# Kernel tuning notes

Hardware: AMD Instinct MI355X
Metric: run time of the kernel (lower is better)

## Reference

```python
import math
import jax, jax.numpy as jnp
import numpy as np

DIM = 1024
QK_DIM = 200
HIDDEN = 2 * DIM  # expansion_factor = 2
N = 8192


def setup_inputs() -> dict:
    key = jax.random.key(0)
    ks = jax.random.split(key, 8)
    s = 0.02
    return {
        "x": jax.random.normal(ks[0], (N, DIM), dtype=jnp.float32),
        "W_hidden": jax.random.normal(ks[1], (DIM, 2 * HIDDEN), dtype=jnp.float32) * s,
        "b_hidden": jnp.zeros((2 * HIDDEN,), dtype=jnp.float32),
        "W_qk": jax.random.normal(ks[2], (DIM, QK_DIM), dtype=jnp.float32) * s,
        "b_qk": jnp.zeros((QK_DIM,), dtype=jnp.float32),
        "gamma": 1.0 + jax.random.normal(ks[3], (2, QK_DIM), dtype=jnp.float32) * s,
        "beta": jnp.zeros((2, QK_DIM), dtype=jnp.float32),
        "W_out": jax.random.normal(ks[4], (HIDDEN, DIM), dtype=jnp.float32) * s,
        "b_out": jnp.zeros((DIM,), dtype=jnp.float32),
    }


def reference(x, W_hidden, b_hidden, W_qk, b_qk, gamma, beta, W_out, b_out):
    # to_hidden: Linear(dim -> 2*hidden) + SiLU, then chunk into v, gate
    hid = jax.nn.silu(x @ W_hidden + b_hidden)        # [N, 2H]
    v, gate = jnp.split(hid, 2, axis=-1)              # [N, H] each
    # to_qk: Linear(dim -> qk_dim) + SiLU
    qk = jax.nn.silu(x @ W_qk + b_qk)                 # [N, qk]
    # OffsetScale (heads=2): per-head affine on the shared qk
    q = qk * gamma[0] + beta[0]                       # [N, qk]
    k = qk * gamma[1] + beta[1]                       # [N, qk]
    # scores scaled by sqrt(dim) (module uses self.dim, not qk_dim)
    sim = (q @ k.T) * (1.0 / math.sqrt(x.shape[-1]))  # [N, N]
    # ReLU-squared attention (no softmax); dropout=0.0 -> identity
    attn = jnp.square(jax.nn.relu(sim))
    out = attn @ v                                    # [N, H]
    out = out * gate
    out = out @ W_out + b_out                         # [N, dim]
    # add_residual=True in this module multiplies by x
    return out * x
```

## Files before the change

kernel.cpp:

```cpp
#include <hip/hip_runtime.h>
#include <stdint.h>


typedef __bf16 bf16x8 __attribute__((ext_vector_type(8)));
typedef float f32x4 __attribute__((ext_vector_type(4)));

__device__ __forceinline__ uint16_t f2bf(float f) {
  uint32_t u = __builtin_bit_cast(uint32_t, f);
  u += 0x7fffu + ((u >> 16) & 1u);
  return (uint16_t)(u >> 16);
}
__device__ __forceinline__ float silu_f(float s) {
  return s / (1.f + __expf(-s));
}

__device__ __forceinline__ void gload16(const void* g, void* l) {
  __builtin_amdgcn_global_load_lds(
      (__attribute__((address_space(1))) void*)const_cast<void*>(g),
      (__attribute__((address_space(3))) void*)l, 16, 0, 0);
}


__global__ void cast_to_bf16(const float* __restrict__ in, uint16_t* __restrict__ out, int n4) {
  int i = blockIdx.x * blockDim.x + threadIdx.x;
  if (i < n4) {
    float4 f = ((const float4*)in)[i];
    ushort4 o;
    o.x = f2bf(f.x); o.y = f2bf(f.y); o.z = f2bf(f.z); o.w = f2bf(f.w);
    ((ushort4*)out)[i] = o;
  }
}

__global__ void transpose_cast_pad(const float* __restrict__ in, uint16_t* __restrict__ out,
                                   int R, int C, int Cp) {
  __shared__ float tile[32][33];
  int cb = blockIdx.x * 32;
  int rb = blockIdx.y * 32;
  int tx = threadIdx.x;
  int ty = threadIdx.y;
#pragma unroll
  for (int i = 0; i < 4; ++i) {
    int r = rb + ty + i * 8;
    int c = cb + tx;
    tile[ty + i * 8][tx] = (c < C) ? in[(size_t)r * C + c] : 0.f;
  }
  __syncthreads();
#pragma unroll
  for (int i = 0; i < 4; ++i) {
    int c = cb + ty + i * 8;
    if (c < Cp) out[(size_t)c * R + rb + tx] = f2bf(tile[tx][ty + i * 8]);
  }
}

__global__ void k_sum(uint16_t* __restrict__ P0, const uint16_t* __restrict__ P1,
                      const uint16_t* __restrict__ g, int n8) {
  int i = blockIdx.x * blockDim.x + threadIdx.x;
  if (i < n8) {
    bf16x8 a = ((const bf16x8*)P0)[i];
    bf16x8 b = ((const bf16x8*)P1)[i];
    bf16x8 gg = ((const bf16x8*)g)[i];
    bf16x8 o;
#pragma unroll
    for (int e = 0; e < 8; ++e)
      o[e] = (__bf16)(((float)a[e] + (float)b[e]) * (float)gg[e]);
    ((bf16x8*)P0)[i] = o;
  }
}


struct EpiParams {
  const float* bias;
  const float* bias2;
  const float* g0;
  const float* b0;
  const float* g1;
  const float* b1;
  const uint16_t* gate;
  const float* x;
  uint16_t* o16a;
  uint16_t* o16b;
  uint16_t* oq;
  uint16_t* ok;
  float* o32;
};

#define TILE128(T_, B_, BS_)                                                   \
  do {                                                                         \
    const uint16_t* base_ = SH + (B_) * 8192;                                  \
    const int kp_ = (((T_) + 3) & (NT - 1)) * 32;                              \
    uint16_t* sd_ = SH + (BS_) * 8192 + wave * 512;                            \
    gload16(gA0 + kp_, sd_);                                                   \
    gload16(gA1 + kp_, sd_ + 2048);                                            \
    gload16(gB0 + kp_, sd_ + 4096);                                            \
    gload16(gB1 + kp_, sd_ + 6144);                                            \
    bf16x8 a_[4], b_[4];                                                       \
    _Pragma("unroll") for (int j = 0; j < 4; ++j)                              \
        b_[j] = *(const bf16x8*)(base_ + rdB + j * 512);                       \
    _Pragma("unroll") for (int i = 0; i < 4; ++i)                              \
        a_[i] = *(const bf16x8*)(base_ + rdA + i * 512);                       \
    __builtin_amdgcn_s_setprio(1);                                             \
    _Pragma("unroll") for (int i = 0; i < 4; ++i)                              \
      _Pragma("unroll") for (int j = 0; j < 4; ++j)                            \
          acc[i][j] = __builtin_amdgcn_mfma_f32_16x16x32_bf16(                 \
              a_[i], b_[j], acc[i][j], 0, 0, 0);                               \
    __builtin_amdgcn_s_setprio(0);                                             \
    asm volatile("s_waitcnt vmcnt(8)" ::: "memory");                           \
    __builtin_amdgcn_sched_barrier(0);                                         \
    __builtin_amdgcn_s_barrier();                                              \
    __builtin_amdgcn_sched_barrier(0);                                         \
  } while (0)

#define RING_LOOP128()                                                         \
  do {                                                                         \
    _Pragma("unroll") for (int s_ = 0; s_ < 3; ++s_) {                         \
      uint16_t* d_ = SH + s_ * 8192 + wave * 512;                              \
      gload16(gA0 + s_ * 32, d_);                                              \
      gload16(gA1 + s_ * 32, d_ + 2048);                                       \
      gload16(gB0 + s_ * 32, d_ + 4096);                                       \
      gload16(gB1 + s_ * 32, d_ + 6144);                                       \
    }                                                                          \
    asm volatile("s_waitcnt vmcnt(8)" ::: "memory");                           \
    __builtin_amdgcn_sched_barrier(0);                                         \
    __builtin_amdgcn_s_barrier();                                              \
    __builtin_amdgcn_sched_barrier(0);                                         \
    for (int t0_ = 0; t0_ < NT; t0_ += 4) {                                    \
      TILE128(t0_ + 0, 0, 3);                                                  \
      TILE128(t0_ + 1, 1, 0);                                                  \
      TILE128(t0_ + 2, 2, 1);                                                  \
      TILE128(t0_ + 3, 3, 2);                                                  \
    }                                                                          \
    asm volatile("s_waitcnt vmcnt(0)" ::: "memory");                           \
    __builtin_amdgcn_sched_barrier(0);                                         \
    __syncthreads();                                                           \
  } while (0)

__global__ __launch_bounds__(256, 2) void k_hidqk(
    const uint16_t* __restrict__ A, const uint16_t* __restrict__ Bt, EpiParams p) {
  __shared__ __align__(16) uint16_t SH[32768];

  const int tid = threadIdx.x;
  const int lane = tid & 63;
  const int wave = tid >> 6;
  const int wr = (wave >> 1) * 64;
  const int wc = (wave & 1) * 64;
  const int m0 = blockIdx.y * 128;
  const int n0 = blockIdx.x * 128;
  const int lda = 1024, ldb = 1024;
  const int NT = 32;

  f32x4 acc[4][4] = {};

  const int fr = lane & 15;
  const int rg = lane >> 4;
  const int swz = (rg ^ ((fr >> 1) & 3)) * 8;
  const int rdA = (wr + fr) * 32 + swz;
  const int rdB = 4096 + (wc + fr) * 32 + swz;

  const int srow = lane >> 2;
  const int sk = ((lane & 3) ^ ((lane >> 3) & 3)) * 8;
  const uint16_t* gA0 = A + (size_t)(m0 + wave * 16 + srow) * lda + sk;
  const uint16_t* gA1 = gA0 + (size_t)64 * lda;
  const uint16_t* gB0 = Bt + (size_t)(n0 + wave * 16 + srow) * ldb + sk;
  const uint16_t* gB1 = gB0 + (size_t)64 * ldb;

  RING_LOOP128();

  if (n0 < 2048) {
    uint16_t* ar = SH + wave * 2048;
    const int lrow = lane >> 3;
    const int mc = (lane & 7) * 8;
#pragma unroll
    for (int j = 0; j < 4; ++j) {
      const float bc = p.bias[n0 + wc + j * 16 + fr];
#pragma unroll
      for (int i = 0; i < 4; ++i)
#pragma unroll
        for (int r = 0; r < 4; ++r)
          ar[fr * 72 + i * 16 + rg * 4 + r] = f2bf(silu_f(acc[i][j][r] + bc));
#pragma unroll
      for (int rr = 0; rr < 2; ++rr) {
        bf16x8 v = *(const bf16x8*)(ar + (rr * 8 + lrow) * 72 + mc);
        *(bf16x8*)(p.o16a + (size_t)(n0 + wc + j * 16 + rr * 8 + lrow) * 8192 + m0 + wr + mc) = v;
      }
    }
  } else if (n0 < 4096) {
    uint16_t* ar = SH + wave * 2048;
    const int lrow = lane >> 3;
    const int nc = (lane & 7) * 8;
    float bc[4];
#pragma unroll
    for (int j = 0; j < 4; ++j) bc[j] = p.bias[n0 + wc + j * 16 + fr];
#pragma unroll
    for (int i = 0; i < 4; ++i) {
#pragma unroll
      for (int j = 0; j < 4; ++j)
#pragma unroll
        for (int r = 0; r < 4; ++r)
          ar[(rg * 4 + r) * 72 + j * 16 + fr] = f2bf(silu_f(acc[i][j][r] + bc[j]));
#pragma unroll
      for (int rr = 0; rr < 2; ++rr) {
        bf16x8 v = *(const bf16x8*)(ar + (rr * 8 + lrow) * 72 + nc);
        *(bf16x8*)(p.o16b + (size_t)(m0 + wr + i * 16 + rr * 8 + lrow) * 2048 + (n0 - 2048) + wc + nc) = v;
      }
    }
  } else {
#pragma unroll
    for (int i = 0; i < 4; ++i) {
#pragma unroll
      for (int j = 0; j < 4; ++j) {
        const int row = m0 + wr + i * 16 + rg * 4;
        const int qc = n0 + wc + j * 16 + fr - 4096;
#pragma unroll
        for (int r = 0; r < 4; ++r) {
          float qv = 0.f, kv = 0.f;
          if (qc < 200) {
            float s = silu_f(acc[i][j][r] + p.bias2[qc]);
            qv = s * p.g0[qc] + p.b0[qc];
            kv = s * p.g1[qc] + p.b1[qc];
          }
          p.oq[(size_t)(row + r) * 256 + qc] = f2bf(qv);
          p.ok[(size_t)(row + r) * 256 + qc] = f2bf(kv);
        }
      }
    }
  }
}

__global__ __launch_bounds__(256, 2) void k_attn(
    const uint16_t* __restrict__ Q,
    const uint16_t* __restrict__ Kt,
    uint16_t* __restrict__ attn) {
  __shared__ __align__(16) uint16_t SH[32768];

  const int tid = threadIdx.x;
  const int lane = tid & 63;
  const int wave = tid >> 6;
  const int wr = (wave >> 1) * 64;
  const int wc = (wave & 1) * 64;
  const int m0 = blockIdx.y * 128;
  const int n0 = blockIdx.x * 128;
  const int lda = 256, ldb = 256;
  const int NT = 8;

  f32x4 acc[4][4] = {};

  const int fr = lane & 15;
  const int rg = lane >> 4;
  const int swz = (rg ^ ((fr >> 1) & 3)) * 8;
  const int rdA = (wr + fr) * 32 + swz;
  const int rdB = 4096 + (wc + fr) * 32 + swz;

  const int srow = lane >> 2;
  const int sk = ((lane & 3) ^ ((lane >> 3) & 3)) * 8;
  const uint16_t* gA0 = Q + (size_t)(m0 + wave * 16 + srow) * lda + sk;
  const uint16_t* gA1 = gA0 + (size_t)64 * lda;
  const uint16_t* gB0 = Kt + (size_t)(n0 + wave * 16 + srow) * ldb + sk;
  const uint16_t* gB1 = gB0 + (size_t)64 * ldb;

  RING_LOOP128();

#pragma unroll
  for (int i = 0; i < 4; ++i) {
    uint16_t* sl = SH + wave * 4096 + (i & 1) * 2048;
#pragma unroll
    for (int j = 0; j < 4; ++j)
#pragma unroll
      for (int r = 0; r < 4; ++r) {
        float s = fmaxf(acc[i][j][r] * 0.03125f, 0.f);
        sl[(rg * 4 + r) * 72 + j * 16 + fr] = f2bf(s * s);
      }
    const int row = lane >> 2;
    const int c0 = (lane & 3) * 16;
    bf16x8 v0 = *(const bf16x8*)(sl + row * 72 + c0);
    bf16x8 v1 = *(const bf16x8*)(sl + row * 72 + c0 + 8);
    uint16_t* dst = attn + (size_t)(m0 + wr + i * 16 + row) * 8192 + (n0 + wc + c0);
    *(bf16x8*)(dst) = v0;
    *(bf16x8*)(dst + 8) = v1;
  }
}

__global__ __launch_bounds__(512, 2) void k_pv(
    const uint16_t* __restrict__ A,
    const uint16_t* __restrict__ Bt,
    uint16_t* __restrict__ P0,
    uint16_t* __restrict__ P1) {
  __shared__ __align__(16) uint16_t SH[65536];

  const int id = blockIdx.x;
  const int bx = id & 7;
  const int kh = (id >> 3) & 1;
  const int by = id >> 4;
  const int m0 = by * 256;
  const int n0 = bx * 256;
  const int kv0 = kh * 4096;

  const int tid = threadIdx.x;
  const int lane = tid & 63;
  const int wave = tid >> 6;
  const int wrM = (wave >> 2) * 128;
  const int wcN = (wave & 3) * 64;

  const int fr = lane & 15;
  const int rg = lane >> 4;
  const int swz = (rg ^ ((fr >> 1) & 3)) * 8;

  const int rdA = (wrM + fr) * 32 + swz;
  const int rdB = 8192 + (wcN + fr) * 32 + swz;

  const int srow = lane >> 2;
  const int sk = ((lane & 3) ^ ((lane >> 3) & 3)) * 8;
  const uint16_t* gA0 = A + (size_t)(m0 + wave * 16 + srow) * 8192 + kv0 + sk;
  const uint16_t* gA1 = gA0 + (size_t)128 * 8192;
  const uint16_t* gB0 = Bt + (size_t)(n0 + wave * 16 + srow) * 8192 + kv0 + sk;
  const uint16_t* gB1 = gB0 + (size_t)128 * 8192;

  f32x4 acc[8][4] = {};
  const int NT = 128;

  for (int s = 0; s < 3; ++s) {
    const int ko = s * 32;
    uint16_t* d = SH + s * 16384 + wave * 512;
    gload16(gA0 + ko, d);
    gload16(gA1 + ko, d + 4096);
    gload16(gB0 + ko, d + 8192);
    gload16(gB1 + ko, d + 12288);
  }
  asm volatile("s_waitcnt vmcnt(8)" ::: "memory");
  __builtin_amdgcn_sched_barrier(0);
  __builtin_amdgcn_s_barrier();
  __builtin_amdgcn_sched_barrier(0);

#define PV_TILE(T_, B_, BS_)                                                   \
  do {                                                                         \
    const uint16_t* bA_ = SH + (B_) * 16384;                                   \
    const int kp_ = (((T_) + 3) & (NT - 1)) * 32;                              \
    uint16_t* sd_ = SH + (BS_) * 16384 + wave * 512;                           \
    gload16(gA0 + kp_, sd_);                                                   \
    gload16(gA1 + kp_, sd_ + 4096);                                            \
    gload16(gB0 + kp_, sd_ + 8192);                                            \
    gload16(gB1 + kp_, sd_ + 12288);                                           \
    bf16x8 aq[8], bq[4];                                                       \
    _Pragma("unroll") for (int j = 0; j < 4; ++j)                              \
        bq[j] = *(const bf16x8*)(bA_ + rdB + j * 512);                         \
    _Pragma("unroll") for (int i = 0; i < 8; ++i)                              \
        aq[i] = *(const bf16x8*)(bA_ + rdA + i * 512);                         \
    __builtin_amdgcn_s_setprio(1);                                             \
    _Pragma("unroll") for (int i = 0; i < 8; ++i)                              \
      _Pragma("unroll") for (int j = 0; j < 4; ++j)                            \
          acc[i][j] = __builtin_amdgcn_mfma_f32_16x16x32_bf16(                 \
              aq[i], bq[j], acc[i][j], 0, 0, 0);                               \
    __builtin_amdgcn_s_setprio(0);                                             \
    asm volatile("s_waitcnt vmcnt(8)" ::: "memory");                           \
    __builtin_amdgcn_sched_barrier(0);                                         \
    __builtin_amdgcn_s_barrier();                                              \
    __builtin_amdgcn_sched_barrier(0);                                         \
  } while (0)

  for (int t0 = 0; t0 < NT; t0 += 4) {
    PV_TILE(t0 + 0, 0, 3);
    PV_TILE(t0 + 1, 1, 0);
    PV_TILE(t0 + 2, 2, 1);
    PV_TILE(t0 + 3, 3, 2);
  }
#undef PV_TILE

  asm volatile("s_waitcnt vmcnt(0)" ::: "memory");
  __builtin_amdgcn_sched_barrier(0);
  __builtin_amdgcn_s_barrier();
  __builtin_amdgcn_sched_barrier(0);

  uint16_t* dst = kh ? P1 : P0;
  uint16_t* ar = SH + wave * 2048;
  const int lrow = lane >> 3;
  const int nc = (lane & 7) * 8;
#pragma unroll
  for (int i = 0; i < 8; ++i) {
#pragma unroll
    for (int j = 0; j < 4; ++j)
#pragma unroll
      for (int r = 0; r < 4; ++r)
        ar[(rg * 4 + r) * 72 + j * 16 + fr] = f2bf(acc[i][j][r]);
#pragma unroll
    for (int rr = 0; rr < 2; ++rr) {
      const size_t base = (size_t)(m0 + wrM + i * 16 + rr * 8 + lrow) * 2048 + n0 + wcN + nc;
      bf16x8 v = *(const bf16x8*)(ar + (rr * 8 + lrow) * 72 + nc);
      *(bf16x8*)(dst + base) = v;
    }
  }
}

__global__ __launch_bounds__(256, 2) void k_final(
    const uint16_t* __restrict__ A,
    const uint16_t* __restrict__ Bt, EpiParams p) {
  __shared__ __align__(16) uint16_t SH[32768];

  const int tid = threadIdx.x;
  const int lane = tid & 63;
  const int wave = tid >> 6;
  const int wr = (wave >> 1) * 64;
  const int wc = (wave & 1) * 64;
  const int m0 = blockIdx.y * 128;
  const int n0 = blockIdx.x * 128;
  const int lda = 2048, ldb = 2048;
  const int NT = 64;

  f32x4 acc[4][4] = {};

  const int fr = lane & 15;
  const int rg = lane >> 4;
  const int swz = (rg ^ ((fr >> 1) & 3)) * 8;
  const int rdA = (wr + fr) * 32 + swz;
  const int rdB = 4096 + (wc + fr) * 32 + swz;

  const int srow = lane >> 2;
  const int sk = ((lane & 3) ^ ((lane >> 3) & 3)) * 8;
  const uint16_t* gA0 = A + (size_t)(m0 + wave * 16 + srow) * lda + sk;
  const uint16_t* gA1 = gA0 + (size_t)64 * lda;
  const uint16_t* gB0 = Bt + (size_t)(n0 + wave * 16 + srow) * ldb + sk;
  const uint16_t* gB1 = gB0 + (size_t)64 * ldb;

  RING_LOOP128();

#pragma unroll
  for (int i = 0; i < 4; ++i) {
#pragma unroll
    for (int j = 0; j < 4; ++j) {
      const int row = m0 + wr + i * 16 + rg * 4;
      const int col = n0 + wc + j * 16 + fr;
      const float bc = p.bias[col];
#pragma unroll
      for (int r = 0; r < 4; ++r) {
        size_t idx = (size_t)(row + r) * 1024 + col;
        p.o32[idx] = (acc[i][j][r] + bc) * p.x[idx];
      }
    }
  }
}


extern "C" void kernel_launch(void* const* d_in, const int* in_sizes, int n_in,
                              void* d_out, int out_size, void* d_ws, size_t ws_size,
                              hipStream_t stream) {
  const float* x        = (const float*)d_in[0];
  const float* W_hidden = (const float*)d_in[1];
  const float* b_hidden = (const float*)d_in[2];
  const float* W_qk     = (const float*)d_in[3];
  const float* b_qk     = (const float*)d_in[4];
  const float* gamma    = (const float*)d_in[5];
  const float* beta     = (const float*)d_in[6];
  const float* W_out    = (const float*)d_in[7];
  const float* b_out    = (const float*)d_in[8];
  float* out = (float*)d_out;

  char* base = (char*)d_ws;
  uint16_t* xb    = (uint16_t*)(base);
  uint16_t* WhT   = (uint16_t*)(base + (16ull << 20));
  uint16_t* WqkT  = (uint16_t*)(base + (24ull << 20));
  uint16_t* attnB = (uint16_t*)(base);
  char* tail = base + (64ull << 20);
  uint16_t* WoT   = (uint16_t*)(tail);
  uint16_t* q     = (uint16_t*)(tail + (4ull << 20));
  uint16_t* kk    = (uint16_t*)(tail + (8ull << 20));
  uint16_t* vT    = (uint16_t*)(tail + (12ull << 20));
  uint16_t* gate  = (uint16_t*)(tail + (44ull << 20));
  uint16_t* out2g = (uint16_t*)(tail + (76ull << 20));
  (void)in_sizes; (void)n_in; (void)out_size; (void)ws_size;

  const size_t PH = 4096ull * 2048;

  cast_to_bf16<<<(8192 * 1024 / 4) / 256, 256, 0, stream>>>(x, xb, 8192 * 1024 / 4);
  transpose_cast_pad<<<dim3(4096 / 32, 1024 / 32), dim3(32, 8), 0, stream>>>(W_hidden, WhT, 1024, 4096, 4096);
  transpose_cast_pad<<<dim3(256 / 32, 1024 / 32), dim3(32, 8), 0, stream>>>(W_qk, WqkT, 1024, 200, 256);
  transpose_cast_pad<<<dim3(1024 / 32, 2048 / 32), dim3(32, 8), 0, stream>>>(W_out, WoT, 2048, 1024, 1024);

  {
    EpiParams p{};
    p.bias = b_hidden; p.bias2 = b_qk;
    p.g0 = gamma; p.b0 = beta; p.g1 = gamma + 200; p.b1 = beta + 200;
    p.o16a = vT; p.o16b = gate; p.oq = q; p.ok = kk;
    k_hidqk<<<dim3(34, 64), 256, 0, stream>>>(xb, WhT, p);
  }

  for (int s = 0; s < 2; ++s) {
    k_attn<<<dim3(64, 32), 256, 0, stream>>>(q + (size_t)s * 4096 * 256, kk, attnB);

    uint16_t* Pa = out2g + (size_t)s * PH;
    uint16_t* Pb = out2g + (size_t)(1 - s) * PH;
    k_pv<<<dim3(256), 512, 0, stream>>>(attnB, vT, Pa, Pb);

    k_sum<<<dim3((int)(PH / 8 / 256)), 256, 0, stream>>>(
        Pa, Pb, gate + (size_t)s * PH, (int)(PH / 8));

    EpiParams p{};
    p.bias = b_out;
    p.x = x + (size_t)s * 4096 * 1024;
    p.o32 = out + (size_t)s * 4096 * 1024;
    k_final<<<dim3(8, 32), 256, 0, stream>>>(Pa, WoT, p);
  }
}
```

Baseline: 653.5 us.

## Use 256x256 register-double-buffered GEMM engine and full-M attention path

Introduces a shared 256x256-tile GEMM main loop that double-buffers LDS fragments in registers, so the LDS reads for the next k-step overlap with the current MFMAs. k_hidqk and k_attn move from 128x128 tiles to this engine. When the workspace is large enough, the whole 8192x8192 attention matrix is computed in one pass and PV runs without the K-split, with the gate multiply fused into the PV epilogue, removing k_sum and the per-half launches. The cost is more registers and LDS per block and a dependence on workspace size to pick the path.

```diff
diff --git a/kernel.cpp b/kernel.cpp
--- a/kernel.cpp
+++ b/kernel.cpp
@@ -84,6 +84,60 @@
   float* o32;
 };
 
+#define ET(T_, WS_, RS_, CA_, CB_, NA_, NB_)                                   \
+  do {                                                                         \
+    const int kp_ = (((T_) + 3) & (NT - 1)) * 32;                              \
+    uint16_t* sd_ = SH + (WS_) * 16384 + wave * 512;                           \
+    gload16(gA0 + kp_, sd_);                                                   \
+    gload16(gA1 + kp_, sd_ + 4096);                                            \
+    gload16(gB0 + kp_, sd_ + 8192);                                            \
+    gload16(gB1 + kp_, sd_ + 12288);                                           \
+    const uint16_t* rb_ = SH + (RS_) * 16384;                                  \
+    _Pragma("unroll") for (int j_ = 0; j_ < 4; ++j_)                           \
+        NB_[j_] = *(const bf16x8*)(rb_ + rdB + j_ * 512);                      \
+    _Pragma("unroll") for (int i_ = 0; i_ < 8; ++i_)                           \
+        NA_[i_] = *(const bf16x8*)(rb_ + rdA + i_ * 512);                      \
+    __builtin_amdgcn_sched_barrier(0);                                         \
+    __builtin_amdgcn_s_setprio(1);                                             \
+    _Pragma("unroll") for (int i_ = 0; i_ < 8; ++i_)                           \
+      _Pragma("unroll") for (int j_ = 0; j_ < 4; ++j_)                         \
+          acc[i_][j_] = __builtin_amdgcn_mfma_f32_16x16x32_bf16(               \
+              CA_[i_], CB_[j_], acc[i_][j_], 0, 0, 0);                         \
+    __builtin_amdgcn_s_setprio(0);                                             \
+    asm volatile("s_waitcnt vmcnt(4)" ::: "memory");                           \
+    __builtin_amdgcn_sched_barrier(0);                                         \
+    __builtin_amdgcn_s_barrier();                                              \
+    __builtin_amdgcn_sched_barrier(0);                                         \
+  } while (0)
+
+#define ENGINE256()                                                            \
+  do {                                                                         \
+    _Pragma("unroll") for (int s_ = 0; s_ < 3; ++s_) {                         \
+      uint16_t* d_ = SH + s_ * 16384 + wave * 512;                             \
+      gload16(gA0 + s_ * 32, d_);                                              \
+      gload16(gA1 + s_ * 32, d_ + 4096);                                       \
+      gload16(gB0 + s_ * 32, d_ + 8192);                                       \
+      gload16(gB1 + s_ * 32, d_ + 12288);                                      \
+    }                                                                          \
+    asm volatile("s_waitcnt vmcnt(4)" ::: "memory");                           \
+    __builtin_amdgcn_sched_barrier(0);                                         \
+    __builtin_amdgcn_s_barrier();                                              \
+    __builtin_amdgcn_sched_barrier(0);                                         \
+    _Pragma("unroll") for (int j_ = 0; j_ < 4; ++j_)                           \
+        fb0[j_] = *(const bf16x8*)(SH + rdB + j_ * 512);                       \
+    _Pragma("unroll") for (int i_ = 0; i_ < 8; ++i_)                           \
+        fa0[i_] = *(const bf16x8*)(SH + rdA + i_ * 512);                       \
+    for (int t0_ = 0; t0_ < NT; t0_ += 4) {                                    \
+      ET(t0_ + 0, 3, 1, fa0, fb0, fa1, fb1);                                   \
+      ET(t0_ + 1, 0, 2, fa1, fb1, fa0, fb0);                                   \
+      ET(t0_ + 2, 1, 3, fa0, fb0, fa1, fb1);                                   \
+      ET(t0_ + 3, 2, 0, fa1, fb1, fa0, fb0);                                   \
+    }                                                                          \
+    asm volatile("s_waitcnt vmcnt(0)" ::: "memory");                           \
+    __builtin_amdgcn_sched_barrier(0);                                         \
+    __syncthreads();                                                           \
+  } while (0)
+
 #define TILE128(T_, B_, BS_)                                                   \
   do {                                                                         \
     const uint16_t* base_ = SH + (B_) * 8192;                                  \
@@ -94,15 +148,15 @@
     gload16(gB0 + kp_, sd_ + 4096);                                            \
     gload16(gB1 + kp_, sd_ + 6144);                                            \
     bf16x8 a_[4], b_[4];                                                       \
-    _Pragma("unroll") for (int j = 0; j < 4; ++j)                              \
-        b_[j] = *(const bf16x8*)(base_ + rdB + j * 512);                       \
-    _Pragma("unroll") for (int i = 0; i < 4; ++i)                              \
-        a_[i] = *(const bf16x8*)(base_ + rdA + i * 512);                       \
+    _Pragma("unroll") for (int j_ = 0; j_ < 4; ++j_)                           \
+        b_[j_] = *(const bf16x8*)(base_ + rdB + j_ * 512);                     \
+    _Pragma("unroll") for (int i_ = 0; i_ < 4; ++i_)                           \
+        a_[i_] = *(const bf16x8*)(base_ + rdA + i_ * 512);                     \
     __builtin_amdgcn_s_setprio(1);                                             \
-    _Pragma("unroll") for (int i = 0; i < 4; ++i)                              \
-      _Pragma("unroll") for (int j = 0; j < 4; ++j)                            \
-          acc[i][j] = __builtin_amdgcn_mfma_f32_16x16x32_bf16(                 \
-              a_[i], b_[j], acc[i][j], 0, 0, 0);                               \
+    _Pragma("unroll") for (int i_ = 0; i_ < 4; ++i_)                           \
+      _Pragma("unroll") for (int j_ = 0; j_ < 4; ++j_)                         \
+          acc[i_][j_] = __builtin_amdgcn_mfma_f32_16x16x32_bf16(               \
+              a_[i_], b_[j_], acc[i_][j_], 0, 0, 0);                           \
     __builtin_amdgcn_s_setprio(0);                                             \
     asm volatile("s_waitcnt vmcnt(8)" ::: "memory");                           \
     __builtin_amdgcn_sched_barrier(0);                                         \
@@ -134,53 +188,54 @@
     __syncthreads();                                                           \
   } while (0)
 
-__global__ __launch_bounds__(256, 2) void k_hidqk(
+__global__ __launch_bounds__(512, 2) void k_hidqk(
     const uint16_t* __restrict__ A, const uint16_t* __restrict__ Bt, EpiParams p) {
-  __shared__ __align__(16) uint16_t SH[32768];
+  __shared__ __align__(16) uint16_t SH[65536];
 
   const int tid = threadIdx.x;
   const int lane = tid & 63;
   const int wave = tid >> 6;
-  const int wr = (wave >> 1) * 64;
-  const int wc = (wave & 1) * 64;
-  const int m0 = blockIdx.y * 128;
-  const int n0 = blockIdx.x * 128;
+  const int wrM = (wave >> 2) * 128;
+  const int wcN = (wave & 3) * 64;
+  const int m0 = blockIdx.y * 256;
+  const int n0 = blockIdx.x * 256;
   const int lda = 1024, ldb = 1024;
   const int NT = 32;
 
-  f32x4 acc[4][4] = {};
+  f32x4 acc[8][4] = {};
 
   const int fr = lane & 15;
   const int rg = lane >> 4;
   const int swz = (rg ^ ((fr >> 1) & 3)) * 8;
-  const int rdA = (wr + fr) * 32 + swz;
-  const int rdB = 4096 + (wc + fr) * 32 + swz;
+  const int rdA = (wrM + fr) * 32 + swz;
+  const int rdB = 8192 + (wcN + fr) * 32 + swz;
 
   const int srow = lane >> 2;
   const int sk = ((lane & 3) ^ ((lane >> 3) & 3)) * 8;
   const uint16_t* gA0 = A + (size_t)(m0 + wave * 16 + srow) * lda + sk;
-  const uint16_t* gA1 = gA0 + (size_t)64 * lda;
+  const uint16_t* gA1 = gA0 + (size_t)128 * lda;
   const uint16_t* gB0 = Bt + (size_t)(n0 + wave * 16 + srow) * ldb + sk;
-  const uint16_t* gB1 = gB0 + (size_t)64 * ldb;
-
-  RING_LOOP128();
+  const uint16_t* gB1 = gB0 + (size_t)128 * ldb;
+
+  bf16x8 fa0[8], fb0[4], fa1[8], fb1[4];
+  ENGINE256();
 
   if (n0 < 2048) {
-    uint16_t* ar = SH + wave * 2048;
-    const int lrow = lane >> 3;
-    const int mc = (lane & 7) * 8;
+    uint16_t* ar = SH + wave * 2304;
 #pragma unroll
     for (int j = 0; j < 4; ++j) {
-      const float bc = p.bias[n0 + wc + j * 16 + fr];
-#pragma unroll
-      for (int i = 0; i < 4; ++i)
+      const float bc = p.bias[n0 + wcN + j * 16 + fr];
+#pragma unroll
+      for (int i = 0; i < 8; ++i)
 #pragma unroll
         for (int r = 0; r < 4; ++r)
-          ar[fr * 72 + i * 16 + rg * 4 + r] = f2bf(silu_f(acc[i][j][r] + bc));
-#pragma unroll
-      for (int rr = 0; rr < 2; ++rr) {
-        bf16x8 v = *(const bf16x8*)(ar + (rr * 8 + lrow) * 72 + mc);
-        *(bf16x8*)(p.o16a + (size_t)(n0 + wc + j * 16 + rr * 8 + lrow) * 8192 + m0 + wr + mc) = v;
+          ar[fr * 136 + i * 16 + rg * 4 + r] = f2bf(silu_f(acc[i][j][r] + bc));
+      const int mc = (lane & 15) * 8;
+#pragma unroll
+      for (int it = 0; it < 4; ++it) {
+        const int nrow = it * 4 + (lane >> 4);
+        bf16x8 v = *(const bf16x8*)(ar + nrow * 136 + mc);
+        *(bf16x8*)(p.o16a + (size_t)(n0 + wcN + j * 16 + nrow) * 8192 + m0 + wrM + mc) = v;
       }
     }
   } else if (n0 < 4096) {
@@ -189,9 +244,9 @@
     const int nc = (lane & 7) * 8;
     float bc[4];
 #pragma unroll
-    for (int j = 0; j < 4; ++j) bc[j] = p.bias[n0 + wc + j * 16 + fr];
-#pragma unroll
-    for (int i = 0; i < 4; ++i) {
+    for (int j = 0; j < 4; ++j) bc[j] = p.bias[n0 + wcN + j * 16 + fr];
+#pragma unroll
+    for (int i = 0; i < 8; ++i) {
 #pragma unroll
       for (int j = 0; j < 4; ++j)
 #pragma unroll
@@ -200,16 +255,16 @@
 #pragma unroll
       for (int rr = 0; rr < 2; ++rr) {
         bf16x8 v = *(const bf16x8*)(ar + (rr * 8 + lrow) * 72 + nc);
-        *(bf16x8*)(p.o16b + (size_t)(m0 + wr + i * 16 + rr * 8 + lrow) * 2048 + (n0 - 2048) + wc + nc) = v;
+        *(bf16x8*)(p.o16b + (size_t)(m0 + wrM + i * 16 + rr * 8 + lrow) * 2048 + (n0 - 2048) + wcN + nc) = v;
       }
     }
   } else {
 #pragma unroll
-    for (int i = 0; i < 4; ++i) {
+    for (int i = 0; i < 8; ++i) {
 #pragma unroll
       for (int j = 0; j < 4; ++j) {
-        const int row = m0 + wr + i * 16 + rg * 4;
-        const int qc = n0 + wc + j * 16 + fr - 4096;
+        const int row = m0 + wrM + i * 16 + rg * 4;
+        const int qc = wcN + j * 16 + fr;
 #pragma unroll
         for (int r = 0; r < 4; ++r) {
           float qv = 0.f, kv = 0.f;
@@ -226,84 +281,97 @@
   }
 }
 
-__global__ __launch_bounds__(256, 2) void k_attn(
+__global__ __launch_bounds__(512, 2) void k_attn(
     const uint16_t* __restrict__ Q,
     const uint16_t* __restrict__ Kt,
     uint16_t* __restrict__ attn) {
-  __shared__ __align__(16) uint16_t SH[32768];
-
-  const int tid = threadIdx.x;
-  const int lane = tid & 63;
-  const int wave = tid >> 6;
-  const int wr = (wave >> 1) * 64;
-  const int wc = (wave & 1) * 64;
-  const int m0 = blockIdx.y * 128;
-  const int n0 = blockIdx.x * 128;
-  const int lda = 256, ldb = 256;
-  const int NT = 8;
-
-  f32x4 acc[4][4] = {};
-
-  const int fr = lane & 15;
-  const int rg = lane >> 4;
-  const int swz = (rg ^ ((fr >> 1) & 3)) * 8;
-  const int rdA = (wr + fr) * 32 + swz;
-  const int rdB = 4096 + (wc + fr) * 32 + swz;
-
-  const int srow = lane >> 2;
-  const int sk = ((lane & 3) ^ ((lane >> 3) & 3)) * 8;
-  const uint16_t* gA0 = Q + (size_t)(m0 + wave * 16 + srow) * lda + sk;
-  const uint16_t* gA1 = gA0 + (size_t)64 * lda;
-  const uint16_t* gB0 = Kt + (size_t)(n0 + wave * 16 + srow) * ldb + sk;
-  const uint16_t* gB1 = gB0 + (size_t)64 * ldb;
-
-  RING_LOOP128();
-
-#pragma unroll
-  for (int i = 0; i < 4; ++i) {
-    uint16_t* sl = SH + wave * 4096 + (i & 1) * 2048;
-#pragma unroll
-    for (int j = 0; j < 4; ++j)
-#pragma unroll
-      for (int r = 0; r < 4; ++r) {
-        float s = fmaxf(acc[i][j][r] * 0.03125f, 0.f);
-        sl[(rg * 4 + r) * 72 + j * 16 + fr] = f2bf(s * s);
-      }
-    const int row = lane >> 2;
-    const int c0 = (lane & 3) * 16;
-    bf16x8 v0 = *(const bf16x8*)(sl + row * 72 + c0);
-    bf16x8 v1 = *(const bf16x8*)(sl + row * 72 + c0 + 8);
-    uint16_t* dst = attn + (size_t)(m0 + wr + i * 16 + row) * 8192 + (n0 + wc + c0);
-    *(bf16x8*)(dst) = v0;
-    *(bf16x8*)(dst + 8) = v1;
-  }
-}
-
-__global__ __launch_bounds__(512, 2) void k_pv(
-    const uint16_t* __restrict__ A,
-    const uint16_t* __restrict__ Bt,
-    uint16_t* __restrict__ P0,
-    uint16_t* __restrict__ P1) {
   __shared__ __align__(16) uint16_t SH[65536];
-
-  const int id = blockIdx.x;
-  const int bx = id & 7;
-  const int kh = (id >> 3) & 1;
-  const int by = id >> 4;
-  const int m0 = by * 256;
-  const int n0 = bx * 256;
-  const int kv0 = kh * 4096;
 
   const int tid = threadIdx.x;
   const int lane = tid & 63;
   const int wave = tid >> 6;
   const int wrM = (wave >> 2) * 128;
   const int wcN = (wave & 3) * 64;
+  const int m0 = blockIdx.y * 256;
+  const int n0 = blockIdx.x * 256;
+  const int lda = 256, ldb = 256;
+  const int NT = 8;
+
+  f32x4 acc[8][4] = {};
 
   const int fr = lane & 15;
   const int rg = lane >> 4;
   const int swz = (rg ^ ((fr >> 1) & 3)) * 8;
-
+  const int rdA = (wrM + fr) * 32 + swz;
+  const int rdB = 8192 + (wcN + fr) * 32 + swz;
+
+  const int srow = lane >> 2;
+  const int sk = ((lane & 3) ^ ((lane >> 3) & 3)) * 8;
+  const uint16_t* gA0 = Q + (size_t)(m0 + wave * 16 + srow) * lda + sk;
+  const uint16_t* gA1 = gA0 + (size_t)128 * lda;
+  const uint16_t* gB0 = Kt + (size_t)(n0 + wave * 16 + srow) * ldb + sk;
+  const uint16_t* gB1 = gB0 + (size_t)128 * ldb;
+
+  bf16x8 fa0[8], fb0[4], fa1[8], fb1[4];
+  ENGINE256();
+
+  uint16_t* ar = SH + wave * 2048;
+  const int row = lane >> 2;
+  const int c0 = (lane & 3) * 16;
+#pragma unroll
+  for (int i = 0; i < 8; ++i) {
+#pragma unroll
+    for (int j = 0; j < 4; ++j)
+#pragma unroll
+      for (int r = 0; r < 4; ++r) {
+        float s = fmaxf(acc[i][j][r] * 0.03125f, 0.f);
+        ar[(rg * 4 + r) * 72 + j * 16 + fr] = f2bf(s * s);
+      }
+    bf16x8 v0 = *(const bf16x8*)(ar + row * 72 + c0);
+    bf16x8 v1 = *(const bf16x8*)(ar + row * 72 + c0 + 8);
+    uint16_t* dst = attn + (size_t)(m0 + wrM + i * 16 + row) * 8192 + (n0 + wcN + c0);
+    *(bf16x8*)(dst) = v0;
+    *(bf16x8*)(dst + 8) = v1;
+  }
+}
+
+__global__ __launch_bounds__(512, 2) void k_pv(
+    const uint16_t* __restrict__ A,
+    const uint16_t* __restrict__ Bt,
+    uint16_t* __restrict__ P0,
+    uint16_t* __restrict__ P1,
+    const uint16_t* __restrict__ gate,
+    int split) {
+  __shared__ __align__(16) uint16_t SH[65536];
+
+  const int id = blockIdx.x;
+  int bx, by, kv0, NT;
+  uint16_t* dst;
+  if (split) {
+    bx = id & 7;
+    by = id >> 4;
+    kv0 = ((id >> 3) & 1) * 4096;
+    NT = 128;
+    dst = ((id >> 3) & 1) ? P1 : P0;
+  } else {
+    bx = (id >> 3) & 7;
+    by = (id & 7) + 8 * (id >> 6);
+    kv0 = 0;
+    NT = 256;
+    dst = P0;
+  }
+  const int m0 = by * 256;
+  const int n0 = bx * 256;
+
+  const int tid = threadIdx.x;
+  const int lane = tid & 63;
+  const int wave = tid >> 6;
+  const int wrM = (wave >> 2) * 128;
+  const int wcN = (wave & 3) * 64;
+
+  const int fr = lane & 15;
+  const int rg = lane >> 4;
+  const int swz = (rg ^ ((fr >> 1) & 3)) * 8;
   const int rdA = (wrM + fr) * 32 + swz;
   const int rdB = 8192 + (wcN + fr) * 32 + swz;
 
@@ -315,61 +383,9 @@
   const uint16_t* gB1 = gB0 + (size_t)128 * 8192;
 
   f32x4 acc[8][4] = {};
-  const int NT = 128;
-
-  for (int s = 0; s < 3; ++s) {
-    const int ko = s * 32;
-    uint16_t* d = SH + s * 16384 + wave * 512;
-    gload16(gA0 + ko, d);
-    gload16(gA1 + ko, d + 4096);
-    gload16(gB0 + ko, d + 8192);
-    gload16(gB1 + ko, d + 12288);
-  }
-  asm volatile("s_waitcnt vmcnt(8)" ::: "memory");
-  __builtin_amdgcn_sched_barrier(0);
-  __builtin_amdgcn_s_barrier();
-  __builtin_amdgcn_sched_barrier(0);
-
-#define PV_TILE(T_, B_, BS_)                                                   \
-  do {                                                                         \
-    const uint16_t* bA_ = SH + (B_) * 16384;                                   \
-    const int kp_ = (((T_) + 3) & (NT - 1)) * 32;                              \
-    uint16_t* sd_ = SH + (BS_) * 16384 + wave * 512;                           \
-    gload16(gA0 + kp_, sd_);                                                   \
-    gload16(gA1 + kp_, sd_ + 4096);                                            \
-    gload16(gB0 + kp_, sd_ + 8192);                                            \
-    gload16(gB1 + kp_, sd_ + 12288);                                           \
-    bf16x8 aq[8], bq[4];                                                       \
-    _Pragma("unroll") for (int j = 0; j < 4; ++j)                              \
-        bq[j] = *(const bf16x8*)(bA_ + rdB + j * 512);                         \
-    _Pragma("unroll") for (int i = 0; i < 8; ++i)                              \
-        aq[i] = *(const bf16x8*)(bA_ + rdA + i * 512);                         \
-    __builtin_amdgcn_s_setprio(1);                                             \
-    _Pragma("unroll") for (int i = 0; i < 8; ++i)                              \
-      _Pragma("unroll") for (int j = 0; j < 4; ++j)                            \
-          acc[i][j] = __builtin_amdgcn_mfma_f32_16x16x32_bf16(                 \
-              aq[i], bq[j], acc[i][j], 0, 0, 0);                               \
-    __builtin_amdgcn_s_setprio(0);                                             \
-    asm volatile("s_waitcnt vmcnt(8)" ::: "memory");                           \
-    __builtin_amdgcn_sched_barrier(0);                                         \
-    __builtin_amdgcn_s_barrier();                                              \
-    __builtin_amdgcn_sched_barrier(0);                                         \
-  } while (0)
-
-  for (int t0 = 0; t0 < NT; t0 += 4) {
-    PV_TILE(t0 + 0, 0, 3);
-    PV_TILE(t0 + 1, 1, 0);
-    PV_TILE(t0 + 2, 2, 1);
-    PV_TILE(t0 + 3, 3, 2);
-  }
-#undef PV_TILE
-
-  asm volatile("s_waitcnt vmcnt(0)" ::: "memory");
-  __builtin_amdgcn_sched_barrier(0);
-  __builtin_amdgcn_s_barrier();
-  __builtin_amdgcn_sched_barrier(0);
-
-  uint16_t* dst = kh ? P1 : P0;
+  bf16x8 fa0[8], fb0[4], fa1[8], fb1[4];
+  ENGINE256();
+
   uint16_t* ar = SH + wave * 2048;
   const int lrow = lane >> 3;
   const int nc = (lane & 7) * 8;
@@ -384,7 +400,15 @@
     for (int rr = 0; rr < 2; ++rr) {
       const size_t base = (size_t)(m0 + wrM + i * 16 + rr * 8 + lrow) * 2048 + n0 + wcN + nc;
       bf16x8 v = *(const bf16x8*)(ar + (rr * 8 + lrow) * 72 + nc);
-      *(bf16x8*)(dst + base) = v;
+      if (gate) {
+        bf16x8 g = *(const bf16x8*)(gate + base);
+        bf16x8 o;
+#pragma unroll
+        for (int e = 0; e < 8; ++e) o[e] = (__bf16)((float)v[e] * (float)g[e]);
+        *(bf16x8*)(dst + base) = o;
+      } else {
+        *(bf16x8*)(dst + base) = v;
+      }
     }
   }
 }
@@ -452,21 +476,22 @@
   const float* b_out    = (const float*)d_in[8];
   float* out = (float*)d_out;
 
+  const bool fullM = ws_size >= (236ull << 20);
+  const size_t region0 = fullM ? (128ull << 20) : (64ull << 20);
+
   char* base = (char*)d_ws;
   uint16_t* xb    = (uint16_t*)(base);
   uint16_t* WhT   = (uint16_t*)(base + (16ull << 20));
   uint16_t* WqkT  = (uint16_t*)(base + (24ull << 20));
   uint16_t* attnB = (uint16_t*)(base);
-  char* tail = base + (64ull << 20);
+  char* tail = base + region0;
   uint16_t* WoT   = (uint16_t*)(tail);
   uint16_t* q     = (uint16_t*)(tail + (4ull << 20));
   uint16_t* kk    = (uint16_t*)(tail + (8ull << 20));
   uint16_t* vT    = (uint16_t*)(tail + (12ull << 20));
   uint16_t* gate  = (uint16_t*)(tail + (44ull << 20));
   uint16_t* out2g = (uint16_t*)(tail + (76ull << 20));
-  (void)in_sizes; (void)n_in; (void)out_size; (void)ws_size;
-
-  const size_t PH = 4096ull * 2048;
+  (void)in_sizes; (void)n_in; (void)out_size;
 
   cast_to_bf16<<<(8192 * 1024 / 4) / 256, 256, 0, stream>>>(x, xb, 8192 * 1024 / 4);
   transpose_cast_pad<<<dim3(4096 / 32, 1024 / 32), dim3(32, 8), 0, stream>>>(W_hidden, WhT, 1024, 4096, 4096);
@@ -478,23 +503,29 @@
     p.bias = b_hidden; p.bias2 = b_qk;
     p.g0 = gamma; p.b0 = beta; p.g1 = gamma + 200; p.b1 = beta + 200;
     p.o16a = vT; p.o16b = gate; p.oq = q; p.ok = kk;
-    k_hidqk<<<dim3(34, 64), 256, 0, stream>>>(xb, WhT, p);
-  }
-
-  for (int s = 0; s < 2; ++s) {
-    k_attn<<<dim3(64, 32), 256, 0, stream>>>(q + (size_t)s * 4096 * 256, kk, attnB);
-
-    uint16_t* Pa = out2g + (size_t)s * PH;
-    uint16_t* Pb = out2g + (size_t)(1 - s) * PH;
-    k_pv<<<dim3(256), 512, 0, stream>>>(attnB, vT, Pa, Pb);
-
-    k_sum<<<dim3((int)(PH / 8 / 256)), 256, 0, stream>>>(
-        Pa, Pb, gate + (size_t)s * PH, (int)(PH / 8));
-
+    k_hidqk<<<dim3(17, 32), 512, 0, stream>>>(xb, WhT, p);
+  }
+
+  if (fullM) {
+    k_attn<<<dim3(32, 32), 512, 0, stream>>>(q, kk, attnB);
+    k_pv<<<dim3(256), 512, 0, stream>>>(attnB, vT, out2g, nullptr, gate, 0);
     EpiParams p{};
-    p.bias = b_out;
-    p.x = x + (size_t)s * 4096 * 1024;
-    p.o32 = out + (size_t)s * 4096 * 1024;
-    k_final<<<dim3(8, 32), 256, 0, stream>>>(Pa, WoT, p);
-  }
-}
+    p.bias = b_out; p.x = x; p.o32 = out;
+    k_final<<<dim3(8, 64), 256, 0, stream>>>(out2g, WoT, p);
+  } else {
+    const size_t PH = 4096ull * 2048;
+    for (int s = 0; s < 2; ++s) {
+      k_attn<<<dim3(32, 16), 512, 0, stream>>>(q + (size_t)s * 4096 * 256, kk, attnB);
+      uint16_t* Pa = out2g + (size_t)s * PH;
+      uint16_t* Pb = out2g + (size_t)(1 - s) * PH;
+      k_pv<<<dim3(256), 512, 0, stream>>>(attnB, vT, Pa, Pb, nullptr, 1);
+      k_sum<<<dim3((int)(PH / 8 / 256)), 256, 0, stream>>>(
+          Pa, Pb, gate + (size_t)s * PH, (int)(PH / 8));
+      EpiParams p{};
+      p.bias = b_out;
+      p.x = x + (size_t)s * 4096 * 1024;
+      p.o32 = out + (size_t)s * 4096 * 1024;
+      k_final<<<dim3(8, 32), 256, 0, stream>>>(Pa, WoT, p);
+    }
+  }
+}
```

Result: faster. 607.2 us (-7.1%).
